# Kernel tuning notes

Hardware: AMD Instinct MI355X
Metric: run time of the kernel (lower is better)

Reference implementation:

```python
import jax, jax.numpy as jnp
import numpy as np

N = 16384          # nodes/edges
F = 128            # features per rank
L_MAX = 3
SIZES = [1, 3, 9, 27]   # 3^l components for l = 0..3

def _doublefactorial(n):
    x = 1
    for i in range(1, n + 1, 2):
        x *= i
    return x

def _factorial(n):
    x = 1
    for i in range(1, n + 1):
        x *= i
    return x

def _norm_l1l2l3(l1, l2, l3):
    # even-parity recoupling normalization (verbatim from source)
    J = l1 + l2 + l3
    J1 = J - 2 * l1 - 1
    J2 = J - 2 * l2 - 1
    J3 = J - 2 * l3 - 1
    num = (_factorial(l1) * _factorial(l2) * _doublefactorial(2 * l3 - 1)
           * _factorial((J1 + 1) // 2) * _factorial((J2 + 1) // 2))
    den = (_factorial(l3) * _doublefactorial(J1) * _doublefactorial(J2)
           * _doublefactorial(J3) * _factorial(J // 2))
    return num / den

# All even-parity recoupling paths (l1, l2, l3): triangle inequality + even l1+l2-l3.
PATHS = [(l1, l2, l3)
         for l3 in range(L_MAX + 1)
         for l1 in range(L_MAX + 1)
         for l2 in range(L_MAX + 1)
         if abs(l1 - l2) <= l3 <= l1 + l2 and (l1 + l2 - l3) % 2 == 0]
N_PATHS = len(PATHS)  # == 23 == _get_n_paths(3,3,3)

def setup_inputs() -> dict:
    key = jax.random.key(0)
    k1, k2, k3 = jax.random.split(key, 3)
    x = jax.random.normal(k1, (N, F * sum(SIZES)), dtype=jnp.float32)
    y = jax.random.normal(k2, (N, F * sum(SIZES)), dtype=jnp.float32)
    weights = jax.random.normal(k3, (N_PATHS, F), dtype=jnp.float32)
    return {"x": x, "y": y, "weights": weights}

def _split(t):
    # flat [N, F*40] -> list of [N, F, 3,...,3] (rank-l Cartesian blocks)
    blocks, off = [], 0
    for l, s in enumerate(SIZES):
        blocks.append(t[:, off:off + F * s].reshape((-1, F) + (3,) * l))
        off += F * s
    return blocks

def reference(x, y, weights):
    xs = _split(x)
    ys = _split(y)
    outs = [jnp.zeros((x.shape[0], F) + (3,) * l3, x.dtype) for l3 in range(L_MAX + 1)]
    for p, (l1, l2, l3) in enumerate(PATHS):
        k = (l1 + l2 - l3) // 2          # number of contracted Cartesian indices
        xa = 'abc'[:l1 - k]              # free indices from x
        c = 'uvw'[:k]                    # contracted indices
        yb = 'deg'[:l2 - k]              # free indices from y
        sub = f"nf{xa}{c},nf{c}{yb}->nf{xa}{yb}"
        z = jnp.einsum(sub, xs[l1], ys[l2])           # [N, F, 3^l3]
        w = weights[p].reshape((1, F) + (1,) * l3)    # per-path per-feature weight
        outs[l3] = outs[l3] + jnp.asarray(_norm_l1l2l3(l1, l2, l3), x.dtype) * w * z
    return jnp.concatenate([o.reshape(o.shape[0], -1) for o in outs], axis=1)
```

## Files before the change

kernel.cpp:

```cpp
#include <hip/hip_runtime.h>


#define FF 128
#define ROW 5120

typedef float floatx4 __attribute__((ext_vector_type(4)));

__device__ __constant__ float NORMS[23] = {
    1.0f, 1.0f, 2.0f/3.0f, 0.4f,
    1.0f, 1.0f, 1.0f, 1.0f, 2.0f/3.0f, 2.0f/3.0f,
    1.0f, 0.75f, 1.0f, 1.0f, 1.0f, 1.0f, 0.75f,
    1.0f, 5.0f/9.0f, 5.0f/9.0f, 5.0f/6.0f, 1.0f, 5.0f/6.0f
};

#define GL2LDS(g, l)  __builtin_amdgcn_global_load_lds(                      \
        (const __attribute__((address_space(1))) void*)(g),                  \
        (__attribute__((address_space(3))) void*)(l), 16, 0, 0)

__global__ __launch_bounds__(256, 2) void wtp_kernel(
    const float* __restrict__ x, const float* __restrict__ y,
    const float* __restrict__ w, float* __restrict__ out)
{
    __shared__ float buf[2 * ROW];

    const int tid   = threadIdx.x;
    const int f     = tid & 127;
    const int half  = tid >> 7;
    const int wbase = (tid >> 6) << 8;

    const int n = blockIdx.x;
    const float* xr = x + (size_t)n * ROW;
    const float* yr = y + (size_t)n * ROW;
    float* orow     = out + (size_t)n * ROW;

    #pragma unroll
    for (int i = 0; i < 5; ++i) {
        GL2LDS(xr + i * 1024 + tid * 4, buf + i * 1024 + wbase);
        GL2LDS(yr + i * 1024 + tid * 4, buf + ROW + i * 1024 + wbase);
    }

    float c[23];
    #pragma unroll
    for (int p = 0; p < 23; ++p) c[p] = NORMS[p] * w[p * FF + f];

    asm volatile("s_waitcnt vmcnt(0)" ::: "memory");
    __syncthreads();

    const float* bx = buf;
    const float* by = buf + ROW;
    const float x0 = bx[f], y0 = by[f];
    float x1[3], y1[3], x2[9], y2[9];
    #pragma unroll
    for (int j = 0; j < 3; ++j)  x1[j] = bx[128  + f*3  + j];
    #pragma unroll
    for (int j = 0; j < 3; ++j)  y1[j] = by[128  + f*3  + j];
    #pragma unroll
    for (int j = 0; j < 9; ++j)  x2[j] = bx[512  + f*9  + j];
    #pragma unroll
    for (int j = 0; j < 9; ++j)  y2[j] = by[512  + f*9  + j];

    const float* bx3 = bx + 1664 + f*27;
    const float* by3 = by + 1664 + f*27;

    float o0, o1[3], o2[9], o3[27];

    if (half == 0) {
        {
            float acc = c[0] * (x0 * y0);
            float d3 = 0.f;
            #pragma unroll
            for (int u = 0; u < 3; ++u) d3 += x1[u] * y1[u];
            acc += c[1] * d3;
            float d9 = 0.f;
            #pragma unroll
            for (int t = 0; t < 9; ++t) d9 += x2[t] * y2[t];
            acc += c[2] * d9;
            float d27 = 0.f;
            #pragma unroll
            for (int t = 0; t < 27; ++t) d27 += bx3[t] * by3[t];
            acc += c[3] * d27;
            o0 = acc;
        }
        #pragma unroll
        for (int d = 0; d < 3; ++d) {
            float acc = c[4] * (x0 * y1[d]) + c[5] * (x1[d] * y0);
            float s6 = 0.f, s7 = 0.f, s8 = 0.f, s9 = 0.f;
            #pragma unroll
            for (int u = 0; u < 3; ++u) s6 += x1[u] * y2[u*3 + d];
            #pragma unroll
            for (int u = 0; u < 3; ++u) s7 += x2[d*3 + u] * y1[u];
            #pragma unroll
            for (int t = 0; t < 9; ++t) s8 += x2[t] * by3[t*3 + d];
            #pragma unroll
            for (int t = 0; t < 9; ++t) s9 += bx3[d*9 + t] * y2[t];
            o1[d] = acc + c[6]*s6 + c[7]*s7 + c[8]*s8 + c[9]*s9;
        }
        #pragma unroll
        for (int t = 0; t < 9; ++t) {
            const int a = t / 3, d = t % 3;
            float acc = c[10] * (x0 * y2[t]) + c[11] * (x1[a] * y1[d])
                      + c[13] * (x2[t] * y0);
            float s12 = 0.f, s14 = 0.f, s15 = 0.f, s16 = 0.f;
            #pragma unroll
            for (int u = 0; u < 3; ++u) s12 += x1[u] * by3[u*9 + t];
            #pragma unroll
            for (int u = 0; u < 3; ++u) s14 += x2[a*3 + u] * y2[u*3 + d];
            #pragma unroll
            for (int u = 0; u < 3; ++u) s15 += bx3[t*3 + u] * y1[u];
            #pragma unroll
            for (int s = 0; s < 9; ++s) s16 += bx3[a*9 + s] * by3[s*3 + d];
            o2[t] = acc + c[12]*s12 + c[14]*s14 + c[15]*s15 + c[16]*s16;
        }
    } else {
        #pragma unroll
        for (int q = 0; q < 27; ++q) {
            const int a = q / 9, t9 = q % 9, r = q / 3, e = q % 3;
            float acc = c[17] * (x0 * by3[q]) + c[18] * (x1[a] * y2[t9])
                      + c[19] * (x2[r] * y1[e]) + c[21] * (bx3[q] * y0);
            float s20 = 0.f, s22 = 0.f;
            #pragma unroll
            for (int u = 0; u < 3; ++u) s20 += x2[a*3 + u] * by3[u*9 + t9];
            #pragma unroll
            for (int u = 0; u < 3; ++u) s22 += bx3[r*3 + u] * y2[u*3 + e];
            o3[q] = acc + c[20]*s20 + c[22]*s22;
        }
    }
    __syncthreads();

    if (half == 0) {
        buf[f] = o0;
        #pragma unroll
        for (int d = 0; d < 3; ++d) buf[128 + f*3 + d] = o1[d];
        #pragma unroll
        for (int t = 0; t < 9; ++t) buf[512 + f*9 + t] = o2[t];
    } else {
        #pragma unroll
        for (int q = 0; q < 27; ++q) buf[1664 + f*27 + q] = o3[q];
    }
    __syncthreads();

    #pragma unroll
    for (int i = 0; i < 5; ++i) {
        floatx4 v = *(const floatx4*)(buf + i * 1024 + tid * 4);
        __builtin_nontemporal_store(v, (floatx4*)(orow + i * 1024 + tid * 4));
    }
}

extern "C" void kernel_launch(void* const* d_in, const int* in_sizes, int n_in,
                              void* d_out, int out_size, void* d_ws, size_t ws_size,
                              hipStream_t stream) {
    const float* x = (const float*)d_in[0];
    const float* y = (const float*)d_in[1];
    const float* w = (const float*)d_in[2];
    float* out = (float*)d_out;

    const int n_nodes = in_sizes[0] / ROW;
    dim3 grid(n_nodes), block(256);
    hipLaunchKernelGGL(wtp_kernel, grid, block, 0, stream, x, y, w, out);
}
```

Before: 188.4 us.

## Split each node row across two blocks by feature half

Each node is now handled by two 128-thread blocks, each owning 64 features, instead of one 256-thread block owning all 128. Global load and store offsets are remapped per rank segment through a helper so that each block gathers only its feature slice into half-size LDS. The aim is a finer grid with less LDS per block, giving more resident blocks and better latency hiding. In exchange, each wave's 16-byte accesses now span segment boundaries with scattered offsets, and the weight loads are duplicated across twice as many blocks.

```diff
diff --git a/kernel.cpp b/kernel.cpp
--- a/kernel.cpp
+++ b/kernel.cpp
@@ -3,6 +3,7 @@
 
 #define FF 128
 #define ROW 5120
+#define HALFROW 2560
 
 typedef float floatx4 __attribute__((ext_vector_type(4)));
 
@@ -17,50 +18,63 @@
         (const __attribute__((address_space(1))) void*)(g),                  \
         (__attribute__((address_space(3))) void*)(l), 16, 0, 0)
 
-__global__ __launch_bounds__(256, 2) void wtp_kernel(
+__device__ __forceinline__ int rowoff(int o, int fbase) {
+    if (o < 64)  return fbase       + o;
+    if (o < 256) return 128 + fbase*3  + (o-64);
+    if (o < 832) return 512 + fbase*9  + (o-256);
+    return 1664 + fbase*27 + (o-832);
+}
+
+__global__ __launch_bounds__(128) void wtp_kernel(
     const float* __restrict__ x, const float* __restrict__ y,
     const float* __restrict__ w, float* __restrict__ out)
 {
-    __shared__ float buf[2 * ROW];
+    __shared__ float buf[2 * HALFROW];
 
     const int tid   = threadIdx.x;
-    const int f     = tid & 127;
-    const int half  = tid >> 7;
-    const int wbase = (tid >> 6) << 8;
+    const int f     = tid & 63;
+    const int half  = tid >> 6;
+    const int wbase = half * 256;
 
-    const int n = blockIdx.x;
+    const int n     = blockIdx.x >> 1;
+    const int fbase = (blockIdx.x & 1) << 6;
+
     const float* xr = x + (size_t)n * ROW;
     const float* yr = y + (size_t)n * ROW;
     float* orow     = out + (size_t)n * ROW;
 
+    int goff[5];
+    #pragma unroll
+    for (int i = 0; i < 5; ++i) goff[i] = rowoff(i * 512 + tid * 4, fbase);
+
     #pragma unroll
     for (int i = 0; i < 5; ++i) {
-        GL2LDS(xr + i * 1024 + tid * 4, buf + i * 1024 + wbase);
-        GL2LDS(yr + i * 1024 + tid * 4, buf + ROW + i * 1024 + wbase);
+        GL2LDS(xr + goff[i], buf + i * 512 + wbase);
+        GL2LDS(yr + goff[i], buf + HALFROW + i * 512 + wbase);
     }
 
     float c[23];
     #pragma unroll
-    for (int p = 0; p < 23; ++p) c[p] = NORMS[p] * w[p * FF + f];
+    for (int p = 0; p < 23; ++p) c[p] = NORMS[p] * w[p * FF + fbase + f];
 
     asm volatile("s_waitcnt vmcnt(0)" ::: "memory");
     __syncthreads();
 
     const float* bx = buf;
-    const float* by = buf + ROW;
+    const float* by = buf + HALFROW;
     const float x0 = bx[f], y0 = by[f];
     float x1[3], y1[3], x2[9], y2[9];
     #pragma unroll
-    for (int j = 0; j < 3; ++j)  x1[j] = bx[128  + f*3  + j];
+    for (int j = 0; j < 3; ++j)  x1[j] = bx[64  + f*3 + j];
     #pragma unroll
-    for (int j = 0; j < 3; ++j)  y1[j] = by[128  + f*3  + j];
+    for (int j = 0; j < 3; ++j)  y1[j] = by[64  + f*3 + j];
     #pragma unroll
-    for (int j = 0; j < 9; ++j)  x2[j] = bx[512  + f*9  + j];
+    for (int j = 0; j < 9; ++j)  x2[j] = bx[256 + f*9 + j];
     #pragma unroll
-    for (int j = 0; j < 9; ++j)  y2[j] = by[512  + f*9  + j];
+    for (int j = 0; j < 9; ++j)  y2[j] = by[256 + f*9 + j];
 
-    const float* bx3 = bx + 1664 + f*27;
-    const float* by3 = by + 1664 + f*27;
+    const float* bx3 = bx + 832 + f*27;
+    const float* by3 = by + 832 + f*27;
 
     float o0, o1[3], o2[9], o3[27];
 
@@ -130,19 +144,19 @@
     if (half == 0) {
         buf[f] = o0;
         #pragma unroll
-        for (int d = 0; d < 3; ++d) buf[128 + f*3 + d] = o1[d];
+        for (int d = 0; d < 3; ++d) buf[64  + f*3 + d] = o1[d];
         #pragma unroll
-        for (int t = 0; t < 9; ++t) buf[512 + f*9 + t] = o2[t];
+        for (int t = 0; t < 9; ++t) buf[256 + f*9 + t] = o2[t];
     } else {
         #pragma unroll
-        for (int q = 0; q < 27; ++q) buf[1664 + f*27 + q] = o3[q];
+        for (int q = 0; q < 27; ++q) buf[832 + f*27 + q] = o3[q];
     }
     __syncthreads();
 
     #pragma unroll
     for (int i = 0; i < 5; ++i) {
-        floatx4 v = *(const floatx4*)(buf + i * 1024 + tid * 4);
-        __builtin_nontemporal_store(v, (floatx4*)(orow + i * 1024 + tid * 4));
+        floatx4 v = *(const floatx4*)(buf + i * 512 + tid * 4);
+        __builtin_nontemporal_store(v, (floatx4*)(orow + goff[i]));
     }
 }
 
@@ -155,6 +169,6 @@
     float* out = (float*)d_out;
 
     const int n_nodes = in_sizes[0] / ROW;
-    dim3 grid(n_nodes), block(256);
+    dim3 grid(n_nodes * 2), block(128);
     hipLaunchKernelGGL(wtp_kernel, grid, block, 0, stream, x, y, w, out);
 }
```

New measurement: 178.0 us, median of 2. 1.06x faster.

## Split each node into four single-wavefront blocks over feature quarters, drop barriers

Applied to the files above, without the earlier changes.

Each block now handles one node's 32-feature slice using a single 64-lane wavefront instead of a full node with 256 threads. Global offsets are remapped per rank segment so each wave loads only its quarter into LDS. Because the whole block is one wavefront, the __syncthreads barriers become explicit waitcnt and sched barriers. The grid grows fourfold and each block loads and stores less, which adds launch/scheduling overhead and produces smaller contiguous segments (32-float chunks for rank 0).

```diff
diff --git a/kernel.cpp b/kernel.cpp
--- a/kernel.cpp
+++ b/kernel.cpp
@@ -3,6 +3,7 @@
 
 #define FF 128
 #define ROW 5120
+#define QROW 1280
 
 typedef float floatx4 __attribute__((ext_vector_type(4)));
 
@@ -17,54 +18,65 @@
         (const __attribute__((address_space(1))) void*)(g),                  \
         (__attribute__((address_space(3))) void*)(l), 16, 0, 0)
 
-__global__ __launch_bounds__(256, 2) void wtp_kernel(
+__global__ __launch_bounds__(64, 4) void wtp_kernel(
     const float* __restrict__ x, const float* __restrict__ y,
     const float* __restrict__ w, float* __restrict__ out)
 {
-    __shared__ float buf[2 * ROW];
+    __shared__ float buf[2 * QROW];
 
-    const int tid   = threadIdx.x;
-    const int f     = tid & 127;
-    const int half  = tid >> 7;
-    const int wbase = (tid >> 6) << 8;
+    const int lane  = threadIdx.x;
+    const int f     = lane & 31;
+    const int h     = lane >> 5;
+    const int n     = blockIdx.x >> 2;
+    const int fbase = (blockIdx.x & 3) << 5;
 
-    const int n = blockIdx.x;
     const float* xr = x + (size_t)n * ROW;
     const float* yr = y + (size_t)n * ROW;
     float* orow     = out + (size_t)n * ROW;
 
+    int goff[5];
     #pragma unroll
     for (int i = 0; i < 5; ++i) {
-        GL2LDS(xr + i * 1024 + tid * 4, buf + i * 1024 + wbase);
-        GL2LDS(yr + i * 1024 + tid * 4, buf + ROW + i * 1024 + wbase);
+        const int o = i * 256 + lane * 4;
+        int r;
+        if      (o < 32)  r = fbase         + o;
+        else if (o < 128) r = 128  + fbase*3  + (o - 32);
+        else if (o < 416) r = 512  + fbase*9  + (o - 128);
+        else              r = 1664 + fbase*27 + (o - 416);
+        goff[i] = r;
+    }
+
+    #pragma unroll
+    for (int i = 0; i < 5; ++i) {
+        GL2LDS(xr + goff[i], buf + i * 256);
+        GL2LDS(yr + goff[i], buf + QROW + i * 256);
     }
 
     float c[23];
     #pragma unroll
-    for (int p = 0; p < 23; ++p) c[p] = NORMS[p] * w[p * FF + f];
+    for (int p = 0; p < 23; ++p) c[p] = NORMS[p] * w[p * FF + fbase + f];
 
     asm volatile("s_waitcnt vmcnt(0)" ::: "memory");
-    __syncthreads();
 
     const float* bx = buf;
-    const float* by = buf + ROW;
+    const float* by = buf + QROW;
     const float x0 = bx[f], y0 = by[f];
     float x1[3], y1[3], x2[9], y2[9];
     #pragma unroll
-    for (int j = 0; j < 3; ++j)  x1[j] = bx[128  + f*3  + j];
+    for (int j = 0; j < 3; ++j)  x1[j] = bx[32  + f*3 + j];
     #pragma unroll
-    for (int j = 0; j < 3; ++j)  y1[j] = by[128  + f*3  + j];
+    for (int j = 0; j < 3; ++j)  y1[j] = by[32  + f*3 + j];
     #pragma unroll
-    for (int j = 0; j < 9; ++j)  x2[j] = bx[512  + f*9  + j];
+    for (int j = 0; j < 9; ++j)  x2[j] = bx[128 + f*9 + j];
     #pragma unroll
-    for (int j = 0; j < 9; ++j)  y2[j] = by[512  + f*9  + j];
+    for (int j = 0; j < 9; ++j)  y2[j] = by[128 + f*9 + j];
 
-    const float* bx3 = bx + 1664 + f*27;
-    const float* by3 = by + 1664 + f*27;
+    const float* bx3 = bx + 416 + f*27;
+    const float* by3 = by + 416 + f*27;
 
     float o0, o1[3], o2[9], o3[27];
 
-    if (half == 0) {
+    if (h == 0) {
         {
             float acc = c[0] * (x0 * y0);
             float d3 = 0.f;
@@ -125,24 +137,24 @@
             o3[q] = acc + c[20]*s20 + c[22]*s22;
         }
     }
-    __syncthreads();
 
-    if (half == 0) {
+    if (h == 0) {
         buf[f] = o0;
         #pragma unroll
-        for (int d = 0; d < 3; ++d) buf[128 + f*3 + d] = o1[d];
+        for (int d = 0; d < 3; ++d) buf[32  + f*3 + d] = o1[d];
         #pragma unroll
-        for (int t = 0; t < 9; ++t) buf[512 + f*9 + t] = o2[t];
+        for (int t = 0; t < 9; ++t) buf[128 + f*9 + t] = o2[t];
     } else {
         #pragma unroll
-        for (int q = 0; q < 27; ++q) buf[1664 + f*27 + q] = o3[q];
+        for (int q = 0; q < 27; ++q) buf[416 + f*27 + q] = o3[q];
     }
-    __syncthreads();
+    asm volatile("s_waitcnt lgkmcnt(0)" ::: "memory");
+    __builtin_amdgcn_sched_barrier(0);
 
     #pragma unroll
     for (int i = 0; i < 5; ++i) {
-        floatx4 v = *(const floatx4*)(buf + i * 1024 + tid * 4);
-        __builtin_nontemporal_store(v, (floatx4*)(orow + i * 1024 + tid * 4));
+        floatx4 v = *(const floatx4*)(buf + i * 256 + lane * 4);
+        __builtin_nontemporal_store(v, (floatx4*)(orow + goff[i]));
     }
 }
 
@@ -155,6 +167,6 @@
     float* out = (float*)d_out;
 
     const int n_nodes = in_sizes[0] / ROW;
-    dim3 grid(n_nodes), block(256);
+    dim3 grid(n_nodes * 4), block(64);
     hipLaunchKernelGGL(wtp_kernel, grid, block, 0, stream, x, y, w, out);
 }
```

After: 255.7 us. 1.36x slower.
